# Kernel tuning notes

Hardware: AMD Instinct MI355X
Metric: run time of the kernel (lower is better)

The kernel has to match this reference:

```python
import jax, jax.numpy as jnp
import numpy as np

NUM_CLASSES = 6
STYLE_DIM = 64
NUM_POINTS = 1000
EMBED_DIM = 1024
NUM_ADAPTERS = 256
LN_EPS = 1e-5


def setup_inputs() -> dict:
    key = jax.random.key(0)
    ks = jax.random.split(key, 24)
    B, N = 8, 64
    ef = jax.random.normal(ks[0], (B, N, EMBED_DIM), dtype=jnp.float32)
    class_labels = jax.random.randint(ks[1], (B, N), 0, NUM_CLASSES)
    adapter_ids = jax.random.randint(ks[2], (B, N), 0, NUM_ADAPTERS)

    def lin(k, fan_in, fan_out):
        lim = 1.0 / np.sqrt(fan_in)
        kw, kb = jax.random.split(k)
        w = jax.random.uniform(kw, (fan_in, fan_out), minval=-lim, maxval=lim, dtype=jnp.float32)
        b = jax.random.uniform(kb, (fan_out,), minval=-lim, maxval=lim, dtype=jnp.float32)
        return w, b

    # StyleEncoder: Linear(1024,256), LayerNorm(256), ReLU, Linear(256,64)
    se_w1, se_b1 = lin(ks[3], EMBED_DIM, 256)
    se_gamma = jnp.ones((256,), jnp.float32)
    se_beta = jnp.zeros((256,), jnp.float32)
    se_w2, se_b2 = lin(ks[4], 256, STYLE_DIM)

    # GlobalEntityPrior MLP: (style+3+classes) -> 256 -> 256 -> 19
    in_dim = STYLE_DIM + 3 + NUM_CLASSES
    gep_w1, gep_b1 = lin(ks[5], in_dim, 256)
    gep_w2, gep_b2 = lin(ks[6], 256, 256)
    gep_w3, gep_b3 = lin(ks[7], 256, 19)
    canonical_points = jax.random.normal(ks[8], (NUM_POINTS, 3), dtype=jnp.float32)

    # LocalResidualAdapter tables (torch init is zeros; use small randn for nontrivial test)
    mu_tab = 0.02 * jax.random.normal(ks[9], (NUM_ADAPTERS, NUM_POINTS, 3), dtype=jnp.float32)
    cov_tab = 0.02 * jax.random.normal(ks[10], (NUM_ADAPTERS, NUM_POINTS, 6), dtype=jnp.float32)
    op_tab = 0.02 * jax.random.normal(ks[11], (NUM_ADAPTERS, NUM_POINTS, 1), dtype=jnp.float32)
    sh_tab = 0.02 * jax.random.normal(ks[12], (NUM_ADAPTERS, NUM_POINTS, 9), dtype=jnp.float32)

    return {
        "entity_features": ef, "class_labels": class_labels, "adapter_ids": adapter_ids,
        "se_w1": se_w1, "se_b1": se_b1, "se_gamma": se_gamma, "se_beta": se_beta,
        "se_w2": se_w2, "se_b2": se_b2,
        "canonical_points": canonical_points,
        "gep_w1": gep_w1, "gep_b1": gep_b1, "gep_w2": gep_w2, "gep_b2": gep_b2,
        "gep_w3": gep_w3, "gep_b3": gep_b3,
        "mu_tab": mu_tab, "cov_tab": cov_tab, "op_tab": op_tab, "sh_tab": sh_tab,
    }


def reference(entity_features, class_labels, adapter_ids,
              se_w1, se_b1, se_gamma, se_beta, se_w2, se_b2,
              canonical_points, gep_w1, gep_b1, gep_w2, gep_b2, gep_w3, gep_b3,
              mu_tab, cov_tab, op_tab, sh_tab):
    # --- StyleEncoder ---
    h = entity_features @ se_w1 + se_b1                       # (B,N,256)
    mean = jnp.mean(h, axis=-1, keepdims=True)
    var = jnp.mean((h - mean) ** 2, axis=-1, keepdims=True)
    h = (h - mean) * jax.lax.rsqrt(var + LN_EPS) * se_gamma + se_beta
    h = jax.nn.relu(h)
    style = h @ se_w2 + se_b2                                 # (B,N,style_dim)

    # --- GlobalEntityPrior: first layer decomposed over concat [style, points, onehot] ---
    oh = jax.nn.one_hot(class_labels, NUM_CLASSES, dtype=jnp.float32)  # (B,N,C)
    w_s = gep_w1[:STYLE_DIM]                                  # (style_dim,256)
    w_p = gep_w1[STYLE_DIM:STYLE_DIM + 3]                     # (3,256)
    w_c = gep_w1[STYLE_DIM + 3:]                              # (C,256)
    ent_part = style @ w_s + oh @ w_c + gep_b1                # (B,N,256)
    pt_part = canonical_points @ w_p                          # (P,256)
    h1 = jax.nn.relu(ent_part[:, :, None, :] + pt_part[None, None])  # (B,N,P,256)
    h2 = jax.nn.relu(h1 @ gep_w2 + gep_b2)                    # (B,N,P,256)
    params = h2 @ gep_w3 + gep_b3                             # (B,N,P,19)

    p_mu = params[..., 0:3]
    p_cov = params[..., 3:9]
    p_op = jax.nn.sigmoid(params[..., 9:10])
    p_sh = params[..., 10:]

    # --- LocalResidualAdapter gather (replaces python dict loop) ---
    final_mu = p_mu + mu_tab[adapter_ids]                     # (B,N,P,3)
    final_cov = p_cov + cov_tab[adapter_ids]                  # (B,N,P,6)
    final_op = p_op + op_tab[adapter_ids]                     # (B,N,P,1)
    final_sh = p_sh + sh_tab[adapter_ids]                     # (B,N,P,9)
    return (final_mu, final_cov, final_op, final_sh)
```

## Files before the change

kernel.cpp:

```cpp
#include <hip/hip_runtime.h>

typedef __attribute__((ext_vector_type(8))) short short8;
typedef __attribute__((ext_vector_type(4))) float float4v;
typedef __attribute__((ext_vector_type(16))) float float16v;

#define SDIM 64

#define MU_OFF   0
#define COV_OFF  1536000
#define OP_OFF   4608000
#define SH_OFF   5120000

__device__ __forceinline__ float bf2f(unsigned short u){ return __uint_as_float(((unsigned)u)<<16); }
__device__ __forceinline__ unsigned short f2bf(float f){
  unsigned u = __float_as_uint(f);
  return (unsigned short)((u + 0x7fffu + ((u>>16)&1u)) >> 16);
}
__device__ __forceinline__ unsigned cvt_pk_bf16(float lo, float hi){
  unsigned r; asm("v_cvt_pk_bf16_f32 %0, %1, %2" : "=v"(r) : "v"(lo), "v"(hi)); return r;
}

__global__ __launch_bounds__(256) void kprep(
    const float* __restrict__ se_w1, const float* __restrict__ gep_w2,
    const float* __restrict__ gep_w3, const float* __restrict__ gep_w1,
    const float* __restrict__ cpts,
    unsigned short* __restrict__ w1b, unsigned short* __restrict__ w2t,
    unsigned short* __restrict__ w3p, unsigned short* __restrict__ ptb){
  int idx = blockIdx.x*256 + threadIdx.x;
  if (idx < 262144){ w1b[idx] = f2bf(se_w1[idx]); return; }
  int i1 = idx - 262144;
  if (i1 < 65536){ int n = i1 >> 8, k = i1 & 255; w2t[i1] = f2bf(gep_w2[k*256+n]); return; }
  int i2 = idx - 327680;
  if (i2 < 8192){ int j = i2 >> 8, k = i2 & 255; w3p[i2] = f2bf(j < 19 ? gep_w3[k*19+j] : 0.f); return; }
  int i3 = idx - 335872;
  if (i3 < 256000){ int p = i3 >> 8, k = i3 & 255;
    float v = cpts[p*3+0]*gep_w1[(SDIM+0)*256+k]
            + cpts[p*3+1]*gep_w1[(SDIM+1)*256+k]
            + cpts[p*3+2]*gep_w1[(SDIM+2)*256+k];
    ptb[i3] = f2bf(v);
  }
}

__global__ __launch_bounds__(512, 2) void kmain(
    const float* __restrict__ ef, const int* __restrict__ cls_lab,
    const unsigned short* __restrict__ w1b,
    const float* __restrict__ se_b1, const float* __restrict__ se_gamma,
    const float* __restrict__ se_beta, const float* __restrict__ se_w2,
    const float* __restrict__ se_b2,
    const float* __restrict__ gep_w1, const float* __restrict__ gep_b1,
    const unsigned short* __restrict__ ptb, const unsigned short* __restrict__ w2t,
    const unsigned short* __restrict__ w3p,
    const float* __restrict__ gep_b2, const float* __restrict__ gep_b3,
    const int* __restrict__ adapter_ids,
    const float* __restrict__ mu_tab, const float* __restrict__ cov_tab,
    const float* __restrict__ op_tab, const float* __restrict__ sh_tab,
    float* __restrict__ out){
  __shared__ unsigned short h1L[64*256];
  __shared__ unsigned short w3L[32*256];
  __shared__ float entL[256];
  __shared__ float b2L[256];
  __shared__ float b3L[32];
  __shared__ float pL[64][21];
  int e = blockIdx.x, t = threadIdx.x;
  int lane = t & 63, wid = t >> 6;
  int l16 = lane & 15, kq = lane >> 4;

  {
    float* efF = (float*)h1L;
    float* scr = (float*)w3L;
    ((float2*)efF)[t] = ((const float2*)(ef + (size_t)e*1024))[t];
    if (t < 256) b2L[t] = gep_b2[t];
    if (t < 32) b3L[t] = (t < 19) ? gep_b3[t] : 0.f;
    __syncthreads();
    {
      int o = t & 255, half = t >> 8;
      const float* efH = efF + half*512;
      const unsigned short* wcol = w1b + half*512*256 + o;
      float a0=0.f,a1=0.f,a2=0.f,a3=0.f;
      #pragma unroll 4
      for (int k=0;k<512;k+=4){
        a0 += efH[k]   * bf2f(wcol[(k  )*256]);
        a1 += efH[k+1] * bf2f(wcol[(k+1)*256]);
        a2 += efH[k+2] * bf2f(wcol[(k+2)*256]);
        a3 += efH[k+3] * bf2f(wcol[(k+3)*256]);
      }
      scr[t] = (a0+a1)+(a2+a3);
    }
    __syncthreads();
    float h = 0.f;
    if (t < 256) h = scr[t] + scr[t+256] + se_b1[t];
    float s1 = h, s2 = h*h;
    #pragma unroll
    for (int o=32;o>0;o>>=1){ s1 += __shfl_xor(s1,o,64); s2 += __shfl_xor(s2,o,64); }
    if (lane==0){ scr[1344+wid]=s1; scr[1352+wid]=s2; }
    __syncthreads();
    float S1=0.f, S2=0.f;
    #pragma unroll
    for (int i=0;i<8;i++){ S1 += scr[1344+i]; S2 += scr[1352+i]; }
    float mean = S1*(1.f/256.f);
    float var  = S2*(1.f/256.f) - mean*mean;
    if (t < 256){
      float hn = (h-mean)*rsqrtf(var+1e-5f)*se_gamma[t] + se_beta[t];
      scr[512+t] = fmaxf(hn, 0.f);
    }
    __syncthreads();
    {
      int s = t & 63, q = t >> 6;
      float st = 0.f;
      #pragma unroll 4
      for (int k=q*32;k<q*32+32;k++) st += scr[512+k]*se_w2[k*64+s];
      scr[768 + q*64 + s] = st;
    }
    __syncthreads();
    if (t < 64){
      float v = 0.f;
      #pragma unroll
      for (int q=0;q<8;q++) v += scr[768 + q*64 + t];
      scr[1280+t] = v + se_b2[t];
    }
    __syncthreads();
    if (t < 256){
      int c = cls_lab[e];
      float ep = gep_b1[t] + gep_w1[(SDIM+3+c)*256 + t];
      #pragma unroll 8
      for (int k=0;k<64;k++) ep += scr[1280+k]*gep_w1[k*256+t];
      entL[t] = ep;
    }
    __syncthreads();
  }

  #pragma unroll
  for (int i=0;i<2;i++){
    int g = t + i*512; int row = g>>5; int kg = g&31;
    uint4 v = *(const uint4*)(w3p + row*256 + kg*8);
    int bo = (row*512 + kg*16) ^ ((row&7)<<4);
    *(uint4*)((char*)w3L + bo) = v;
  }
  short8 bB[8][2];
  #pragma unroll
  for (int s=0;s<8;s++)
    #pragma unroll
    for (int r=0;r<2;r++){
      int n  = wid*32 + r*16 + l16;
      int k0 = s*32 + kq*8;
      bB[s][r] = *(const short8*)(w2t + n*256 + k0);
    }
  __syncthreads();

  int aid = adapter_ids[e];
  const float* muT  = mu_tab  + (size_t)aid*3000;
  const float* covT = cov_tab + (size_t)aid*6000;
  const float* opT  = op_tab  + (size_t)aid*1000;
  const float* shT  = sh_tab  + (size_t)aid*9000;
  int kg0 = (t & 31)*8;

  uint4 pv[4];
  #pragma unroll
  for (int i=0;i<4;i++){
    int p = (t>>5) + i*16;
    pv[i] = *(const uint4*)(ptb + p*256 + (t&31)*8);
  }

  for (int c=0;c<16;c++){
    int p0 = c*64;
    int valid = 1000 - p0; if (valid > 64) valid = 64;
    {
      float4v e0 = *(float4v*)&entL[kg0];
      float4v e1 = *(float4v*)&entL[kg0+4];
      #pragma unroll
      for (int i=0;i<4;i++){
        int row = (t>>5) + i*16;
        unsigned pw[4] = {pv[i].x, pv[i].y, pv[i].z, pv[i].w};
        unsigned rw[4];
        #pragma unroll
        for (int w=0; w<4; w++){
          float er0 = (w<2)? e0[2*w]   : e1[2*w-4];
          float er1 = (w<2)? e0[2*w+1] : e1[2*w-3];
          float lo = __uint_as_float(pw[w]<<16);
          float hi = __uint_as_float(pw[w] & 0xffff0000u);
          lo = fmaxf(lo + er0, 0.f); hi = fmaxf(hi + er1, 0.f);
          rw[w] = cvt_pk_bf16(lo, hi);
        }
        int bo = (row*512 + (t&31)*16) ^ ((row&7)<<4);
        *(uint4*)((char*)h1L + bo) = make_uint4(rw[0],rw[1],rw[2],rw[3]);
      }
    }
    __syncthreads();
    {
      int p0n = p0 + 64;
      #pragma unroll
      for (int i=0;i<4;i++){
        int p = p0n + (t>>5) + i*16; p = (p>999)?999:p;
        pv[i] = *(const uint4*)(ptb + p*256 + (t&31)*8);
      }
    }
    float4v acc[4][2];
    #pragma unroll
    for (int m=0;m<4;m++){
      acc[m][0] = (float4v){0.f,0.f,0.f,0.f};
      acc[m][1] = (float4v){0.f,0.f,0.f,0.f};
    }
    #pragma unroll
    for (int s=0;s<8;s++){
      #pragma unroll
      for (int m=0;m<4;m++){
        int row = m*16 + l16;
        int bo = (row*512 + s*64 + kq*16) ^ ((row&7)<<4);
        short8 a = *(const short8*)((char*)h1L + bo);
        acc[m][0] = __builtin_amdgcn_mfma_f32_16x16x32_bf16(bB[s][0], a, acc[m][0], 0,0,0);
        acc[m][1] = __builtin_amdgcn_mfma_f32_16x16x32_bf16(bB[s][1], a, acc[m][1], 0,0,0);
      }
    }
    __syncthreads();
    float tmu=0.f, tcov=0.f, top=0.f, tsh0=0.f, tsh1=0.f;
    if (t < valid*3) tmu  = muT [p0*3 + t];
    if (t < valid*6) tcov = covT[p0*6 + t];
    if (t < valid)   top  = opT [p0 + t];
    if (t < valid*9) tsh0 = shT [p0*9 + t];
    if (t+512 < valid*9) tsh1 = shT[p0*9 + t + 512];
    {
      float4v bias0 = *(float4v*)&b2L[wid*32 + kq*4];
      float4v bias1 = *(float4v*)&b2L[wid*32 + 16 + kq*4];
      #pragma unroll
      for (int m=0;m<4;m++){
        int p = m*16 + l16;
        int rowx = (p&7)<<4;
        #pragma unroll
        for (int r=0;r<2;r++){
          float4v b = r ? bias1 : bias0;
          float v0 = fmaxf(acc[m][r][0]+b[0], 0.f);
          float v1 = fmaxf(acc[m][r][1]+b[1], 0.f);
          float v2 = fmaxf(acc[m][r][2]+b[2], 0.f);
          float v3 = fmaxf(acc[m][r][3]+b[3], 0.f);
          unsigned w0 = cvt_pk_bf16(v0,v1);
          unsigned w1 = cvt_pk_bf16(v2,v3);
          int nbase = wid*32 + r*16 + kq*4;
          int bo = (p*512 + nbase*2) ^ rowx;
          uint2 val; val.x = w0; val.y = w1;
          *(uint2*)((char*)h1L + bo) = val;
        }
      }
    }
    __syncthreads();
    if (wid < 2){
      float16v acc2;
      #pragma unroll
      for (int r=0;r<16;r++) acc2[r] = 0.f;
      int pr = wid*32 + (lane & 31);
      int jr = lane & 31;
      int kb2 = (lane >> 5) * 16;
      int prx = (pr&7)<<4, jrx = (jr&7)<<4;
      #pragma unroll
      for (int s=0;s<16;s++){
        int nb = s*32 + kb2;
        short8 a2 = *(const short8*)((char*)h1L + ((pr*512 + nb) ^ prx));
        short8 bw = *(const short8*)((char*)w3L + ((jr*512 + nb) ^ jrx));
        acc2 = __builtin_amdgcn_mfma_f32_32x32x16_bf16(a2, bw, acc2, 0,0,0);
      }
      if (jr < 19){
        float bj = b3L[jr];
        int pb = wid*32 + 4*(lane>>5);
        #pragma unroll
        for (int r=0;r<16;r++){
          int p_out = pb + (r&3) + 8*(r>>2);
          pL[p_out][jr] = acc2[r] + bj;
        }
      }
    }
    __syncthreads();
    {
      int base = e*1000 + p0;
      if (t < valid*3){
        int p = t/3, cc = t - p*3;
        out[MU_OFF + base*3 + t] = pL[p][cc] + tmu;
      }
      if (t < valid*6){
        int p = t/6, cc = t - p*6;
        out[COV_OFF + base*6 + t] = pL[p][3+cc] + tcov;
      }
      if (t < valid){
        float v = pL[t][9];
        out[OP_OFF + base + t] = 1.f/(1.f+__expf(-v)) + top;
      }
      if (t < valid*9){
        int p = t/9, cc = t - p*9;
        out[SH_OFF + base*9 + t] = pL[p][10+cc] + tsh0;
      }
      if (t+512 < valid*9){
        int idx = t+512; int p = idx/9, cc = idx - p*9;
        out[SH_OFF + base*9 + idx] = pL[p][10+cc] + tsh1;
      }
    }
  }
}

extern "C" void kernel_launch(void* const* d_in, const int* in_sizes, int n_in,
                              void* d_out, int out_size, void* d_ws, size_t ws_size,
                              hipStream_t stream){
  const float* ef    = (const float*)d_in[0];
  const int*   cls   = (const int*)d_in[1];
  const int*   aid   = (const int*)d_in[2];
  const float* se_w1 = (const float*)d_in[3];
  const float* se_b1 = (const float*)d_in[4];
  const float* se_g  = (const float*)d_in[5];
  const float* se_be = (const float*)d_in[6];
  const float* se_w2 = (const float*)d_in[7];
  const float* se_b2 = (const float*)d_in[8];
  const float* cpts  = (const float*)d_in[9];
  const float* gw1   = (const float*)d_in[10];
  const float* gb1   = (const float*)d_in[11];
  const float* gw2   = (const float*)d_in[12];
  const float* gb2   = (const float*)d_in[13];
  const float* gw3   = (const float*)d_in[14];
  const float* gb3   = (const float*)d_in[15];
  const float* mu_t  = (const float*)d_in[16];
  const float* cov_t = (const float*)d_in[17];
  const float* op_t  = (const float*)d_in[18];
  const float* sh_t  = (const float*)d_in[19];
  float* out = (float*)d_out;
  char* ws = (char*)d_ws;
  unsigned short* w1b = (unsigned short*)(ws);
  unsigned short* w2t = (unsigned short*)(ws + 524288);
  unsigned short* w3p = (unsigned short*)(ws + 655360);
  unsigned short* ptb = (unsigned short*)(ws + 671744);

  kprep<<<2312, 256, 0, stream>>>(se_w1, gw2, gw3, gw1, cpts, w1b, w2t, w3p, ptb);
  kmain<<<512, 512, 0, stream>>>(ef, cls, w1b, se_b1, se_g, se_be, se_w2, se_b2,
                                 gw1, gb1, ptb, w2t, w3p, gb2, gb3, aid,
                                 mu_t, cov_t, op_t, sh_t, out);
}
```

Measured before the change: 156.8 us.

## Overlap chunk output epilogue with next chunk's third-layer MFMA via warp specialization

Double-buffers the per-chunk params tile in shared memory. Waves 2-7 write out the previous chunk's results while waves 0-1 run the small third-layer MFMA for the current chunk, which removes one barrier per chunk. The adapter-table loads for the previous chunk are issued earlier and overlap the h1 build. The style-encoder first linear is also restructured so each thread does vectorized 8-column bf16 row loads over a 64-k slice, followed by a 16-way shared reduction, instead of strided scalar column loads. The final partial chunk is handled in a separate tail, which adds complexity and depends on fixed 1000-point indexing.

```diff
diff --git a/kernel.cpp b/kernel.cpp
--- a/kernel.cpp
+++ b/kernel.cpp
@@ -60,35 +60,43 @@
   __shared__ float entL[256];
   __shared__ float b2L[256];
   __shared__ float b3L[32];
-  __shared__ float pL[64][21];
+  __shared__ float pL[2][64][21];
   int e = blockIdx.x, t = threadIdx.x;
   int lane = t & 63, wid = t >> 6;
   int l16 = lane & 15, kq = lane >> 4;
 
   {
     float* efF = (float*)h1L;
+    float* red = (float*)h1L + 1024;
     float* scr = (float*)w3L;
     ((float2*)efF)[t] = ((const float2*)(ef + (size_t)e*1024))[t];
     if (t < 256) b2L[t] = gep_b2[t];
     if (t < 32) b3L[t] = (t < 19) ? gep_b3[t] : 0.f;
     __syncthreads();
     {
-      int o = t & 255, half = t >> 8;
-      const float* efH = efF + half*512;
-      const unsigned short* wcol = w1b + half*512*256 + o;
-      float a0=0.f,a1=0.f,a2=0.f,a3=0.f;
-      #pragma unroll 4
-      for (int k=0;k<512;k+=4){
-        a0 += efH[k]   * bf2f(wcol[(k  )*256]);
-        a1 += efH[k+1] * bf2f(wcol[(k+1)*256]);
-        a2 += efH[k+2] * bf2f(wcol[(k+2)*256]);
-        a3 += efH[k+3] * bf2f(wcol[(k+3)*256]);
-      }
-      scr[t] = (a0+a1)+(a2+a3);
+      int kg = t >> 5, c8 = (t & 31)*8;
+      const unsigned short* wrow = w1b + (kg*64)*256 + c8;
+      float a[8];
+      #pragma unroll
+      for (int j=0;j<8;j++) a[j]=0.f;
+      #pragma unroll 8
+      for (int k=0;k<64;k++){
+        short8 w = *(const short8*)(wrow + k*256);
+        float ev = efF[kg*64 + k];
+        #pragma unroll
+        for (int j=0;j<8;j++) a[j] += ev * bf2f((unsigned short)w[j]);
+      }
+      #pragma unroll
+      for (int j=0;j<8;j++) red[kg*256 + c8 + j] = a[j];
     }
     __syncthreads();
     float h = 0.f;
-    if (t < 256) h = scr[t] + scr[t+256] + se_b1[t];
+    if (t < 256){
+      float s = 0.f;
+      #pragma unroll
+      for (int g=0; g<16; g++) s += red[g*256 + t];
+      h = s + se_b1[t];
+    }
     float s1 = h, s2 = h*h;
     #pragma unroll
     for (int o=32;o>0;o>>=1){ s1 += __shfl_xor(s1,o,64); s2 += __shfl_xor(s2,o,64); }
@@ -161,9 +169,10 @@
     pv[i] = *(const uint4*)(ptb + p*256 + (t&31)*8);
   }
 
+  float tmu=0.f, tcov=0.f, top=0.f, tsh0=0.f, tsh1=0.f;
+
   for (int c=0;c<16;c++){
     int p0 = c*64;
-    int valid = 1000 - p0; if (valid > 64) valid = 64;
     {
       float4v e0 = *(float4v*)&entL[kg0];
       float4v e1 = *(float4v*)&entL[kg0+4];
@@ -185,6 +194,15 @@
         *(uint4*)((char*)h1L + bo) = make_uint4(rw[0],rw[1],rw[2],rw[3]);
       }
     }
+    if (c > 0 && t >= 128){
+      int tt = t - 128;
+      int g0 = (c-1)*64;
+      if (tt < 192) tmu  = muT [g0*3 + tt];
+      if (tt < 384) tcov = covT[g0*6 + tt];
+      if (tt < 64)  top  = opT [g0 + tt];
+      if (tt < 384) tsh0 = shT [g0*9 + tt];
+      if (tt < 192) tsh1 = shT [g0*9 + 384 + tt];
+    }
     __syncthreads();
     {
       int p0n = p0 + 64;
@@ -212,12 +230,6 @@
       }
     }
     __syncthreads();
-    float tmu=0.f, tcov=0.f, top=0.f, tsh0=0.f, tsh1=0.f;
-    if (t < valid*3) tmu  = muT [p0*3 + t];
-    if (t < valid*6) tcov = covT[p0*6 + t];
-    if (t < valid)   top  = opT [p0 + t];
-    if (t < valid*9) tsh0 = shT [p0*9 + t];
-    if (t+512 < valid*9) tsh1 = shT[p0*9 + t + 512];
     {
       float4v bias0 = *(float4v*)&b2L[wid*32 + kq*4];
       float4v bias1 = *(float4v*)&b2L[wid*32 + 16 + kq*4];
@@ -263,34 +275,32 @@
         #pragma unroll
         for (int r=0;r<16;r++){
           int p_out = pb + (r&3) + 8*(r>>2);
-          pL[p_out][jr] = acc2[r] + bj;
+          pL[c&1][p_out][jr] = acc2[r] + bj;
         }
       }
-    }
-    __syncthreads();
-    {
-      int base = e*1000 + p0;
-      if (t < valid*3){
-        int p = t/3, cc = t - p*3;
-        out[MU_OFF + base*3 + t] = pL[p][cc] + tmu;
-      }
-      if (t < valid*6){
-        int p = t/6, cc = t - p*6;
-        out[COV_OFF + base*6 + t] = pL[p][3+cc] + tcov;
-      }
-      if (t < valid){
-        float v = pL[t][9];
-        out[OP_OFF + base + t] = 1.f/(1.f+__expf(-v)) + top;
-      }
-      if (t < valid*9){
-        int p = t/9, cc = t - p*9;
-        out[SH_OFF + base*9 + t] = pL[p][10+cc] + tsh0;
-      }
-      if (t+512 < valid*9){
-        int idx = t+512; int p = idx/9, cc = idx - p*9;
-        out[SH_OFF + base*9 + idx] = pL[p][10+cc] + tsh1;
-      }
-    }
+    } else if (c > 0){
+      int tt = t - 128;
+      int par = (c-1)&1;
+      int base = e*1000 + (c-1)*64;
+      if (tt < 192){ int p=tt/3, q=tt-p*3; out[MU_OFF + base*3 + tt] = pL[par][p][q] + tmu; }
+      if (tt < 384){ int p=tt/6, q=tt-p*6; out[COV_OFF + base*6 + tt] = pL[par][p][3+q] + tcov; }
+      if (tt < 64){ float v = pL[par][tt][9]; out[OP_OFF + base + tt] = 1.f/(1.f+__expf(-v)) + top; }
+      if (tt < 384){ int p=tt/9, q=tt-p*9; out[SH_OFF + base*9 + tt] = pL[par][p][10+q] + tsh0; }
+      if (tt < 192){ int i2=tt+384; int p=i2/9, q=i2-p*9; out[SH_OFF + base*9 + i2] = pL[par][p][10+q] + tsh1; }
+    }
+    __syncthreads();
+  }
+  {
+    int base = e*1000 + 960;
+    float gmu=0.f,gcov=0.f,gop=0.f,gsh=0.f;
+    if (t < 120) gmu  = muT [2880 + t];
+    if (t < 240) gcov = covT[5760 + t];
+    if (t < 40)  gop  = opT [960 + t];
+    if (t < 360) gsh  = shT [8640 + t];
+    if (t < 120){ int p=t/3, q=t-p*3; out[MU_OFF + base*3 + t] = pL[1][p][q] + gmu; }
+    if (t < 240){ int p=t/6, q=t-p*6; out[COV_OFF + base*6 + t] = pL[1][p][3+q] + gcov; }
+    if (t < 40){ float v = pL[1][t][9]; out[OP_OFF + base + t] = 1.f/(1.f+__expf(-v)) + gop; }
+    if (t < 360){ int p=t/9, q=t-p*9; out[SH_OFF + base*9 + t] = pL[1][p][10+q] + gsh; }
   }
 }
 
```

New measurement: 139.0 us. 11.3% less time.
